# Optimization experiments

Measured on AMD Instinct MI355X. Metric: run time of the kernel, lower is better.

## Reference

```python
import jax, jax.numpy as jnp
import numpy as np

B, T, D, H = 2, 2048, 1024, 16
STD = 0.02

def setup_inputs() -> dict:
    key = jax.random.key(0)
    ks = jax.random.split(key, 5)
    x = jax.random.normal(ks[0], (B, T, D), dtype=jnp.float32)
    Wq = jax.random.normal(ks[1], (D, D), dtype=jnp.float32) * STD
    Wk = jax.random.normal(ks[2], (D, D), dtype=jnp.float32) * STD
    Wv = jax.random.normal(ks[3], (D, D), dtype=jnp.float32) * STD
    Wo = jax.random.normal(ks[4], (D, D), dtype=jnp.float32) * STD
    z = jnp.zeros((D,), dtype=jnp.float32)
    return {"x": x, "Wq": Wq, "bq": z, "Wk": Wk, "bk": z, "Wv": Wv, "bv": z, "Wo": Wo, "bo": z}

def _split(t, h):
    b, s, dm = t.shape
    return t.reshape(b, s, h, dm // h).transpose(0, 2, 1, 3)  # (B,h,T,d)

def reference(x, Wq, bq, Wk, bk, Wv, bv, Wo, bo):
    h = H
    # linear projections (nn.Linear: y = x @ W^T + b)
    q = _split(x @ Wq.T + bq, h)
    k = _split(x @ Wk.T + bk, h)
    v = _split(x @ Wv.T + bv, h)
    d_k = k.shape[-1]
    # scaled dot-product similarities (B,h,T,T)
    sim = jnp.einsum("bhqd,bhkd->bhqk", q, k) / jnp.sqrt(jnp.float32(d_k))
    # causal mask: upper triangle (excluding diag) filled with -inf
    Tq = sim.shape[-1]
    causal = jnp.tril(jnp.ones((Tq, Tq), dtype=bool))
    sim = jnp.where(causal, sim, -jnp.inf)
    attn = jax.nn.softmax(sim, axis=-1)
    ctx = jnp.einsum("bhqk,bhkd->bhqd", attn, v)  # (B,h,T,d)
    ctx = ctx.transpose(0, 2, 1, 3).reshape(x.shape[0], x.shape[1], -1)  # (B,T,D)
    return ctx @ Wo.T + bo
```

## Files before the change

kernel.cpp:

```cpp
#include <hip/hip_runtime.h>
#include <hip/hip_bf16.h>


typedef __attribute__((ext_vector_type(8))) short bf16x8;
typedef __attribute__((ext_vector_type(4))) float f32x4;

#define QSCALE 0.18033688011f

__device__ __forceinline__ int sniff_f32(const void* p) {
    const unsigned short* u = (const unsigned short*)p;
    int c = 0;
    for (int i = 0; i < 256; ++i) {
        int e = (u[i] >> 7) & 0xFF;
        c += (e >= 0x90) ? 1 : 0;
    }
    return c > 8;
}

__device__ __forceinline__ void async_copy16(const void* g, void* l) {
    __builtin_amdgcn_global_load_lds(
        (const __attribute__((address_space(1))) void*)g,
        (__attribute__((address_space(3))) void*)l, 16, 0, 0);
}

struct Cvt { const void* src; __hip_bfloat16* dst; int n; };
struct CvtPack { Cvt a[9]; };

__global__ __launch_bounds__(256) void cvt_bf16(CvtPack pk) {
    const Cvt c = pk.a[blockIdx.y];
    const int f32 = sniff_f32(c.src);
    const int stride = gridDim.x * 256 * 8;
    for (int idx = (blockIdx.x * 256 + threadIdx.x) * 8; idx < c.n; idx += stride) {
        if (f32) {
            const float* s = (const float*)c.src + idx;
            f32x4 a0 = *(const f32x4*)s;
            f32x4 a1 = *(const f32x4*)(s + 4);
            union { __hip_bfloat16 h[8]; bf16x8 v; } u;
#pragma unroll
            for (int e = 0; e < 4; e++) u.h[e]     = (__hip_bfloat16)a0[e];
#pragma unroll
            for (int e = 0; e < 4; e++) u.h[4 + e] = (__hip_bfloat16)a1[e];
            *(bf16x8*)&c.dst[idx] = u.v;
        } else {
            *(bf16x8*)&c.dst[idx] = *(const bf16x8*)((const __hip_bfloat16*)c.src + idx);
        }
    }
}

template <bool OF32>
__device__ __forceinline__ void gemm_async_body(
    const __hip_bfloat16* __restrict__ A, const __hip_bfloat16* __restrict__ W,
    const __hip_bfloat16* __restrict__ bias, void* __restrict__ C,
    int M, int N, int K, int bm, int bn, float outscale,
    __hip_bfloat16* sA, __hip_bfloat16* sB)
{
    const int tid  = threadIdx.x;
    const int wave = tid >> 6;
    const int lane = tid & 63;
    const int quad = lane >> 4;
    const int l15  = lane & 15;
    const int wr   = wave >> 1;
    const int wc   = wave & 1;

    const int srow = wave * 16 + (lane >> 2);
    const int scol = (lane & 3) * 8;
    const __hip_bfloat16* gA0 = A + (size_t)(bm + srow) * K + scol;
    const __hip_bfloat16* gB0 = W + (size_t)(bn + srow) * K + scol;
    __hip_bfloat16* sA0 = sA + wave * 512;
    __hip_bfloat16* sB0 = sB + wave * 512;

    f32x4 acc[4][4];
#pragma unroll
    for (int i = 0; i < 4; i++)
#pragma unroll
        for (int j = 0; j < 4; j++) acc[i][j] = (f32x4)0.0f;

    for (int k0 = 0; k0 < K; k0 += 32) {
        __syncthreads();
#pragma unroll
        for (int r = 0; r < 2; r++) {
            async_copy16(gA0 + (size_t)r * 64 * K + k0, sA0 + r * 2048);
            async_copy16(gB0 + (size_t)r * 64 * K + k0, sB0 + r * 2048);
        }
        __syncthreads();

        bf16x8 af[4], bf[4];
#pragma unroll
        for (int i = 0; i < 4; i++)
            af[i] = *(const bf16x8*)&sA[(wr * 64 + i * 16 + l15) * 32 + quad * 8];
#pragma unroll
        for (int j = 0; j < 4; j++)
            bf[j] = *(const bf16x8*)&sB[(wc * 64 + j * 16 + l15) * 32 + quad * 8];
#pragma unroll
        for (int i = 0; i < 4; i++)
#pragma unroll
            for (int j = 0; j < 4; j++)
                acc[i][j] = __builtin_amdgcn_mfma_f32_16x16x32_bf16(af[i], bf[j], acc[i][j], 0, 0, 0);
    }

    float bv[4];
#pragma unroll
    for (int j = 0; j < 4; j++)
        bv[j] = (float)bias[bn + wc * 64 + j * 16 + l15];
#pragma unroll
    for (int i = 0; i < 4; i++) {
#pragma unroll
        for (int j = 0; j < 4; j++) {
            int col = bn + wc * 64 + j * 16 + l15;
#pragma unroll
            for (int r = 0; r < 4; r++) {
                int row = bm + wr * 64 + i * 16 + quad * 4 + r;
                float v = (acc[i][j][r] + bv[j]) * outscale;
                if (OF32) ((float*)C)[(size_t)row * N + col] = v;
                else      ((__hip_bfloat16*)C)[(size_t)row * N + col] = (__hip_bfloat16)v;
            }
        }
    }
}

__global__ __launch_bounds__(256, 2) void qkv_gemm(
    const __hip_bfloat16* __restrict__ x,
    const __hip_bfloat16* __restrict__ Wq, const __hip_bfloat16* __restrict__ bq, __hip_bfloat16* __restrict__ Q,
    const __hip_bfloat16* __restrict__ Wk, const __hip_bfloat16* __restrict__ bk, __hip_bfloat16* __restrict__ Kb,
    const __hip_bfloat16* __restrict__ Wv, const __hip_bfloat16* __restrict__ bv, __hip_bfloat16* __restrict__ V,
    int M, int N, int K)
{
    __shared__ __hip_bfloat16 sA[128 * 32];
    __shared__ __hip_bfloat16 sB[128 * 32];
    const __hip_bfloat16* Wp; const __hip_bfloat16* bp; __hip_bfloat16* Cp; float sc;
    if (blockIdx.z == 0)      { Wp = Wq; bp = bq; Cp = Q;  sc = QSCALE; }
    else if (blockIdx.z == 1) { Wp = Wk; bp = bk; Cp = Kb; sc = 1.0f; }
    else                      { Wp = Wv; bp = bv; Cp = V;  sc = 1.0f; }
    gemm_async_body<false>(x, Wp, bp, Cp, M, N, K,
                           blockIdx.x * 128, blockIdx.y * 128, sc, sA, sB);
}

template <bool OF32>
__device__ __forceinline__ void gemm64_body(
    const __hip_bfloat16* __restrict__ A, const __hip_bfloat16* __restrict__ W,
    const __hip_bfloat16* __restrict__ bias, void* __restrict__ C,
    int M, int N, int K, int bm, int bn,
    __hip_bfloat16* sA, __hip_bfloat16* sB)
{
    const int tid  = threadIdx.x;
    const int wave = tid >> 6;
    const int lane = tid & 63;
    const int quad = lane >> 4;
    const int l15  = lane & 15;

    const int srow = wave * 16 + (lane >> 2);
    const int scol = (lane & 3) * 8;
    const __hip_bfloat16* gA0 = A + (size_t)(bm + srow) * K + scol;
    const __hip_bfloat16* gB0 = W + (size_t)(bn + srow) * K + scol;
    __hip_bfloat16* sA0 = sA + wave * 512;
    __hip_bfloat16* sB0 = sB + wave * 512;

    f32x4 acc[4][2];
#pragma unroll
    for (int i = 0; i < 4; i++)
#pragma unroll
        for (int j = 0; j < 2; j++) acc[i][j] = (f32x4)0.0f;

    for (int k0 = 0; k0 < K; k0 += 32) {
        __syncthreads();
        async_copy16(gA0 + k0, sA0);
#pragma unroll
        for (int r = 0; r < 2; r++)
            async_copy16(gB0 + (size_t)r * 64 * K + k0, sB0 + r * 2048);
        __syncthreads();

        bf16x8 af[4], bf[2];
#pragma unroll
        for (int i = 0; i < 4; i++)
            af[i] = *(const bf16x8*)&sA[(i * 16 + l15) * 32 + quad * 8];
#pragma unroll
        for (int j = 0; j < 2; j++)
            bf[j] = *(const bf16x8*)&sB[(wave * 32 + j * 16 + l15) * 32 + quad * 8];
#pragma unroll
        for (int i = 0; i < 4; i++)
#pragma unroll
            for (int j = 0; j < 2; j++)
                acc[i][j] = __builtin_amdgcn_mfma_f32_16x16x32_bf16(af[i], bf[j], acc[i][j], 0, 0, 0);
    }

    float bv[2];
#pragma unroll
    for (int j = 0; j < 2; j++)
        bv[j] = (float)bias[bn + wave * 32 + j * 16 + l15];
#pragma unroll
    for (int i = 0; i < 4; i++) {
#pragma unroll
        for (int j = 0; j < 2; j++) {
            int col = bn + wave * 32 + j * 16 + l15;
#pragma unroll
            for (int r = 0; r < 4; r++) {
                int row = bm + i * 16 + quad * 4 + r;
                float v = acc[i][j][r] + bv[j];
                if (OF32) ((float*)C)[(size_t)row * N + col] = v;
                else      ((__hip_bfloat16*)C)[(size_t)row * N + col] = (__hip_bfloat16)v;
            }
        }
    }
}

__global__ __launch_bounds__(256, 2) void out_gemm(
    const __hip_bfloat16* __restrict__ A, const __hip_bfloat16* __restrict__ W,
    const __hip_bfloat16* __restrict__ bias, const void* __restrict__ origW,
    void* __restrict__ C, int M, int N, int K)
{
    __shared__ __hip_bfloat16 sA[64 * 32];
    __shared__ __hip_bfloat16 sB[128 * 32];
    __shared__ int f32flag;
    if (threadIdx.x == 0) f32flag = sniff_f32(origW);
    __syncthreads();
    if (f32flag)
        gemm64_body<true>(A, W, bias, C, M, N, K, blockIdx.x * 64, blockIdx.y * 128, sA, sB);
    else
        gemm64_body<false>(A, W, bias, C, M, N, K, blockIdx.x * 64, blockIdx.y * 128, sA, sB);
}

__global__ __launch_bounds__(256, 2) void transpose_v(
    const __hip_bfloat16* __restrict__ V, __hip_bfloat16* __restrict__ VT,
    int T, int D, int H)
{
    __shared__ __hip_bfloat16 sT[64 * 72];
    const int tid = threadIdx.x;
    const int t0  = blockIdx.x * 64;
    const int h   = blockIdx.y;
    const int b   = blockIdx.z;

    for (int i = tid; i < 512; i += 256) {
        int t = i >> 3, d8 = (i & 7) * 8;
        *(bf16x8*)&sT[t * 72 + d8] =
            *(const bf16x8*)&V[((size_t)b * T + t0 + t) * D + h * 64 + d8];
    }
    __syncthreads();
    for (int i = tid; i < 512; i += 256) {
        int d = i >> 3, t8 = (i & 7) * 8;
        union { __hip_bfloat16 h[8]; bf16x8 v; } u;
#pragma unroll
        for (int e = 0; e < 8; e++) u.h[e] = sT[(t8 + e) * 72 + d];
        *(bf16x8*)&VT[(((size_t)b * H + h) * 64 + d) * T + t0 + t8] = u.v;
    }
}

#define PAD 68

__global__ __launch_bounds__(256, 2) void attn_causal(
    const __hip_bfloat16* __restrict__ Q,
    const __hip_bfloat16* __restrict__ K,
    const __hip_bfloat16* __restrict__ VT,
    __hip_bfloat16* __restrict__ O,
    int T, int D, int H)
{
    __shared__ __hip_bfloat16 sK[64 * PAD];
    __shared__ __hip_bfloat16 sVT[64 * PAD];
    __shared__ __hip_bfloat16 sP[4][32 * PAD];

    const int tid  = threadIdx.x;
    const int wave = tid >> 6;
    const int lane = tid & 63;
    const int quad = lane >> 4;
    const int l15  = lane & 15;

    const int NT = T >> 7;
    const int qt = blockIdx.z ? (NT - 1 - (int)blockIdx.x) : (int)blockIdx.x;
    const int h  = blockIdx.y;
    const int b  = blockIdx.z;
    const size_t headoff = (size_t)b * T * D + (size_t)h * 64;
    const size_t vtoff   = ((size_t)b * H + h) * 64 * (size_t)T;

    const int nkt = 2 * qt + 2;
    const int myrowmax = qt * 128 + wave * 32 + 31;

    bf16x8 qfrag[2][2];
#pragma unroll
    for (int g = 0; g < 2; g++)
#pragma unroll
        for (int kk = 0; kk < 2; kk++)
            qfrag[g][kk] = *(const bf16x8*)&Q[headoff +
                (size_t)(qt * 128 + wave * 32 + g * 16 + l15) * D + kk * 32 + quad * 8];

    f32x4 acc_o[2][4];
#pragma unroll
    for (int g = 0; g < 2; g++)
#pragma unroll
        for (int j = 0; j < 4; j++) acc_o[g][j] = (f32x4)0.0f;
    float lacc[2][4] = {{0.f,0.f,0.f,0.f},{0.f,0.f,0.f,0.f}};

    const int srow = tid >> 3;
    const int sc8  = (tid & 7) * 8;

    bf16x8 pk[2], pv[2];
#pragma unroll
    for (int u = 0; u < 2; u++) {
        int row = srow + u * 32;
        pk[u] = *(const bf16x8*)&K[headoff + (size_t)row * D + sc8];
        pv[u] = *(const bf16x8*)&VT[vtoff + (size_t)row * T + sc8];
    }

    for (int kt = 0; kt < nkt; ++kt) {
        __syncthreads();
#pragma unroll
        for (int u = 0; u < 2; u++) {
            int row = srow + u * 32;
            *(bf16x8*)&sK[row * PAD + sc8]  = pk[u];
            *(bf16x8*)&sVT[row * PAD + sc8] = pv[u];
        }
        if (kt + 1 < nkt) {
#pragma unroll
            for (int u = 0; u < 2; u++) {
                int row = srow + u * 32;
                pk[u] = *(const bf16x8*)&K[headoff + (size_t)((kt + 1) * 64 + row) * D + sc8];
                pv[u] = *(const bf16x8*)&VT[vtoff + (size_t)row * T + (kt + 1) * 64 + sc8];
            }
        }
        __syncthreads();

        if (kt * 64 > myrowmax) continue;

        bf16x8 kfrag[2][4], vfrag[2][4];
#pragma unroll
        for (int kk = 0; kk < 2; kk++)
#pragma unroll
            for (int j = 0; j < 4; j++) {
                kfrag[kk][j] = *(const bf16x8*)&sK[(j * 16 + l15) * PAD + kk * 32 + quad * 8];
                vfrag[kk][j] = *(const bf16x8*)&sVT[(j * 16 + l15) * PAD + kk * 32 + quad * 8];
            }

        const int needmask = (kt * 64 + 63 > qt * 128 + wave * 32 + quad * 4);

#pragma unroll
        for (int g = 0; g < 2; g++) {
            f32x4 s[4];
#pragma unroll
            for (int j = 0; j < 4; j++) s[j] = (f32x4)0.0f;
#pragma unroll
            for (int kk = 0; kk < 2; kk++)
#pragma unroll
                for (int j = 0; j < 4; j++)
                    s[j] = __builtin_amdgcn_mfma_f32_16x16x32_bf16(qfrag[g][kk], kfrag[kk][j], s[j], 0, 0, 0);

            if (needmask) {
                const int qrow = qt * 128 + wave * 32 + g * 16 + quad * 4;
#pragma unroll
                for (int j = 0; j < 4; j++) {
                    int key = kt * 64 + j * 16 + l15;
#pragma unroll
                    for (int r = 0; r < 4; r++)
                        if (key > qrow + r) s[j][r] = -1e30f;
                }
            }

#pragma unroll
            for (int j = 0; j < 4; j++) {
#pragma unroll
                for (int r = 0; r < 4; r++) {
                    float p = exp2f(s[j][r]);
                    lacc[g][r] += p;
                    sP[wave][(g * 16 + quad * 4 + r) * PAD + j * 16 + l15] = (__hip_bfloat16)p;
                }
            }
        }
#pragma unroll
        for (int g = 0; g < 2; g++)
#pragma unroll
            for (int kk = 0; kk < 2; kk++) {
                bf16x8 a = *(const bf16x8*)&sP[wave][(g * 16 + l15) * PAD + kk * 32 + quad * 8];
#pragma unroll
                for (int j = 0; j < 4; j++)
                    acc_o[g][j] = __builtin_amdgcn_mfma_f32_16x16x32_bf16(a, vfrag[kk][j], acc_o[g][j], 0, 0, 0);
            }
    }

#pragma unroll
    for (int o = 1; o < 16; o <<= 1)
#pragma unroll
        for (int g = 0; g < 2; g++)
#pragma unroll
            for (int r = 0; r < 4; r++)
                lacc[g][r] += __shfl_xor(lacc[g][r], o, 64);

#pragma unroll
    for (int g = 0; g < 2; g++)
#pragma unroll
        for (int r = 0; r < 4; r++) {
            float inv = 1.0f / lacc[g][r];
            int row = qt * 128 + wave * 32 + g * 16 + quad * 4 + r;
#pragma unroll
            for (int j = 0; j < 4; j++) {
                int col = j * 16 + l15;
                O[headoff + (size_t)row * D + col] = (__hip_bfloat16)(acc_o[g][j][r] * inv);
            }
        }
}

extern "C" void kernel_launch(void* const* d_in, const int* in_sizes, int n_in,
                              void* d_out, int out_size, void* d_ws, size_t ws_size,
                              hipStream_t stream) {
    const int Bb = 2, T = 2048, D = 1024, H = 16;
    const int M = Bb * T;

    __hip_bfloat16* w = (__hip_bfloat16*)d_ws;
    __hip_bfloat16* Q   = w;
    __hip_bfloat16* Kb  = Q   + (size_t)M * D;
    __hip_bfloat16* Vb  = Kb  + (size_t)M * D;
    __hip_bfloat16* ctx = Vb  + (size_t)M * D;
    __hip_bfloat16* VT  = ctx + (size_t)M * D;
    __hip_bfloat16* xb  = VT  + (size_t)M * D;
    __hip_bfloat16* Wqb = xb  + (size_t)M * D;
    __hip_bfloat16* Wkb = Wqb + (size_t)D * D;
    __hip_bfloat16* Wvb = Wkb + (size_t)D * D;
    __hip_bfloat16* Wob = Wvb + (size_t)D * D;
    __hip_bfloat16* bqb = Wob + (size_t)D * D;
    __hip_bfloat16* bkb = bqb + D;
    __hip_bfloat16* bvb = bkb + D;
    __hip_bfloat16* bob = bvb + D;

    CvtPack pk;
    pk.a[0] = { d_in[0], xb,  M * D };
    pk.a[1] = { d_in[1], Wqb, D * D };
    pk.a[2] = { d_in[2], bqb, D };
    pk.a[3] = { d_in[3], Wkb, D * D };
    pk.a[4] = { d_in[4], bkb, D };
    pk.a[5] = { d_in[5], Wvb, D * D };
    pk.a[6] = { d_in[6], bvb, D };
    pk.a[7] = { d_in[7], Wob, D * D };
    pk.a[8] = { d_in[8], bob, D };

    cvt_bf16<<<dim3(512, 9), 256, 0, stream>>>(pk);
    qkv_gemm<<<dim3(M / 128, D / 128, 3), 256, 0, stream>>>(
        xb, Wqb, bqb, Q, Wkb, bkb, Kb, Wvb, bvb, Vb, M, D, D);
    transpose_v<<<dim3(T / 64, H, Bb), 256, 0, stream>>>(Vb, VT, T, D, H);
    attn_causal<<<dim3(T / 128, H, Bb), 256, 0, stream>>>(Q, Kb, VT, ctx, T, D, H);
    out_gemm<<<dim3(M / 64, D / 128), 256, 0, stream>>>(
        ctx, Wob, bob, d_in[7], d_out, M, D, D);
}
```

Measured before the change: 222.9 us.

## Fuse V transpose into QKV GEMM epilogue and double-buffer attention K/V tiles

The V projection epilogue now writes V directly in the transposed per-head layout, which removes the separate transpose_v kernel and its extra round trip through global memory. The attention kernel double-buffers K and V^T in shared memory so only one barrier is needed per tile. It also computes S transposed (K as the A operand), which allows vectorized 4-wide stores of P and a per-lane row-sum reduction with fewer shuffles. The cost is twice the shared memory for the K/V tiles and scattered 8-byte stores in the V epilogue.

```diff
diff --git a/kernel.cpp b/kernel.cpp
--- a/kernel.cpp
+++ b/kernel.cpp
@@ -4,6 +4,7 @@
 
 typedef __attribute__((ext_vector_type(8))) short bf16x8;
 typedef __attribute__((ext_vector_type(4))) float f32x4;
+typedef __attribute__((ext_vector_type(4))) short s16x4;
 
 #define QSCALE 0.18033688011f
 
@@ -47,7 +48,7 @@
     }
 }
 
-template <bool OF32>
+template <int MODE>
 __device__ __forceinline__ void gemm_async_body(
     const __hip_bfloat16* __restrict__ A, const __hip_bfloat16* __restrict__ W,
     const __hip_bfloat16* __restrict__ bias, void* __restrict__ C,
@@ -102,17 +103,37 @@
 #pragma unroll
     for (int j = 0; j < 4; j++)
         bv[j] = (float)bias[bn + wc * 64 + j * 16 + l15];
-#pragma unroll
-    for (int i = 0; i < 4; i++) {
-#pragma unroll
-        for (int j = 0; j < 4; j++) {
-            int col = bn + wc * 64 + j * 16 + l15;
-#pragma unroll
-            for (int r = 0; r < 4; r++) {
-                int row = bm + wr * 64 + i * 16 + quad * 4 + r;
-                float v = (acc[i][j][r] + bv[j]) * outscale;
-                if (OF32) ((float*)C)[(size_t)row * N + col] = v;
-                else      ((__hip_bfloat16*)C)[(size_t)row * N + col] = (__hip_bfloat16)v;
+
+    if (MODE == 2) {
+        __hip_bfloat16* VTo = (__hip_bfloat16*)C;
+#pragma unroll
+        for (int i = 0; i < 4; i++) {
+            int tglob = bm + wr * 64 + i * 16 + quad * 4;
+            int bb = tglob >> 11, tt = tglob & 2047;
+#pragma unroll
+            for (int j = 0; j < 4; j++) {
+                int d = bn + wc * 64 + j * 16 + l15;
+                int hh = d >> 6, dh = d & 63;
+                union { __hip_bfloat16 e[4]; s16x4 v; } u;
+#pragma unroll
+                for (int r = 0; r < 4; r++)
+                    u.e[r] = (__hip_bfloat16)(acc[i][j][r] + bv[j]);
+                *(s16x4*)&VTo[(((size_t)bb * 16 + hh) * 64 + dh) * 2048 + tt] = u.v;
+            }
+        }
+    } else {
+#pragma unroll
+        for (int i = 0; i < 4; i++) {
+#pragma unroll
+            for (int j = 0; j < 4; j++) {
+                int col = bn + wc * 64 + j * 16 + l15;
+#pragma unroll
+                for (int r = 0; r < 4; r++) {
+                    int row = bm + wr * 64 + i * 16 + quad * 4 + r;
+                    float v = (acc[i][j][r] + bv[j]) * outscale;
+                    if (MODE == 1) ((float*)C)[(size_t)row * N + col] = v;
+                    else ((__hip_bfloat16*)C)[(size_t)row * N + col] = (__hip_bfloat16)v;
+                }
             }
         }
     }
@@ -122,17 +143,17 @@
     const __hip_bfloat16* __restrict__ x,
     const __hip_bfloat16* __restrict__ Wq, const __hip_bfloat16* __restrict__ bq, __hip_bfloat16* __restrict__ Q,
     const __hip_bfloat16* __restrict__ Wk, const __hip_bfloat16* __restrict__ bk, __hip_bfloat16* __restrict__ Kb,
-    const __hip_bfloat16* __restrict__ Wv, const __hip_bfloat16* __restrict__ bv, __hip_bfloat16* __restrict__ V,
+    const __hip_bfloat16* __restrict__ Wv, const __hip_bfloat16* __restrict__ bv, __hip_bfloat16* __restrict__ VT,
     int M, int N, int K)
 {
     __shared__ __hip_bfloat16 sA[128 * 32];
     __shared__ __hip_bfloat16 sB[128 * 32];
-    const __hip_bfloat16* Wp; const __hip_bfloat16* bp; __hip_bfloat16* Cp; float sc;
-    if (blockIdx.z == 0)      { Wp = Wq; bp = bq; Cp = Q;  sc = QSCALE; }
-    else if (blockIdx.z == 1) { Wp = Wk; bp = bk; Cp = Kb; sc = 1.0f; }
-    else                      { Wp = Wv; bp = bv; Cp = V;  sc = 1.0f; }
-    gemm_async_body<false>(x, Wp, bp, Cp, M, N, K,
-                           blockIdx.x * 128, blockIdx.y * 128, sc, sA, sB);
+    if (blockIdx.z == 0)
+        gemm_async_body<0>(x, Wq, bq, Q, M, N, K, blockIdx.x * 128, blockIdx.y * 128, QSCALE, sA, sB);
+    else if (blockIdx.z == 1)
+        gemm_async_body<0>(x, Wk, bk, Kb, M, N, K, blockIdx.x * 128, blockIdx.y * 128, 1.0f, sA, sB);
+    else
+        gemm_async_body<2>(x, Wv, bv, VT, M, N, K, blockIdx.x * 128, blockIdx.y * 128, 1.0f, sA, sB);
 }
 
 template <bool OF32>
@@ -219,31 +240,6 @@
         gemm64_body<false>(A, W, bias, C, M, N, K, blockIdx.x * 64, blockIdx.y * 128, sA, sB);
 }
 
-__global__ __launch_bounds__(256, 2) void transpose_v(
-    const __hip_bfloat16* __restrict__ V, __hip_bfloat16* __restrict__ VT,
-    int T, int D, int H)
-{
-    __shared__ __hip_bfloat16 sT[64 * 72];
-    const int tid = threadIdx.x;
-    const int t0  = blockIdx.x * 64;
-    const int h   = blockIdx.y;
-    const int b   = blockIdx.z;
-
-    for (int i = tid; i < 512; i += 256) {
-        int t = i >> 3, d8 = (i & 7) * 8;
-        *(bf16x8*)&sT[t * 72 + d8] =
-            *(const bf16x8*)&V[((size_t)b * T + t0 + t) * D + h * 64 + d8];
-    }
-    __syncthreads();
-    for (int i = tid; i < 512; i += 256) {
-        int d = i >> 3, t8 = (i & 7) * 8;
-        union { __hip_bfloat16 h[8]; bf16x8 v; } u;
-#pragma unroll
-        for (int e = 0; e < 8; e++) u.h[e] = sT[(t8 + e) * 72 + d];
-        *(bf16x8*)&VT[(((size_t)b * H + h) * 64 + d) * T + t0 + t8] = u.v;
-    }
-}
-
 #define PAD 68
 
 __global__ __launch_bounds__(256, 2) void attn_causal(
@@ -253,9 +249,9 @@
     __hip_bfloat16* __restrict__ O,
     int T, int D, int H)
 {
-    __shared__ __hip_bfloat16 sK[64 * PAD];
-    __shared__ __hip_bfloat16 sVT[64 * PAD];
-    __shared__ __hip_bfloat16 sP[4][32 * PAD];
+    __shared__ __hip_bfloat16 sK[2][64 * PAD];
+    __shared__ __hip_bfloat16 sVT[2][64 * PAD];
+    __shared__ __hip_bfloat16 sPA[4][32 * PAD];
 
     const int tid  = threadIdx.x;
     const int wave = tid >> 6;
@@ -286,7 +282,7 @@
     for (int g = 0; g < 2; g++)
 #pragma unroll
         for (int j = 0; j < 4; j++) acc_o[g][j] = (f32x4)0.0f;
-    float lacc[2][4] = {{0.f,0.f,0.f,0.f},{0.f,0.f,0.f,0.f}};
+    float lacc[2] = {0.f, 0.f};
 
     const int srow = tid >> 3;
     const int sc8  = (tid & 7) * 8;
@@ -298,99 +294,119 @@
         pk[u] = *(const bf16x8*)&K[headoff + (size_t)row * D + sc8];
         pv[u] = *(const bf16x8*)&VT[vtoff + (size_t)row * T + sc8];
     }
-
-    for (int kt = 0; kt < nkt; ++kt) {
-        __syncthreads();
+#pragma unroll
+    for (int u = 0; u < 2; u++) {
+        int row = srow + u * 32;
+        *(bf16x8*)&sK[0][row * PAD + sc8]  = pk[u];
+        *(bf16x8*)&sVT[0][row * PAD + sc8] = pv[u];
+    }
+    if (nkt > 1) {
 #pragma unroll
         for (int u = 0; u < 2; u++) {
             int row = srow + u * 32;
-            *(bf16x8*)&sK[row * PAD + sc8]  = pk[u];
-            *(bf16x8*)&sVT[row * PAD + sc8] = pv[u];
-        }
+            pk[u] = *(const bf16x8*)&K[headoff + (size_t)(64 + row) * D + sc8];
+            pv[u] = *(const bf16x8*)&VT[vtoff + (size_t)row * T + 64 + sc8];
+        }
+    }
+    __syncthreads();
+
+    for (int kt = 0; kt < nkt; ++kt) {
+        const int cur = kt & 1;
+
         if (kt + 1 < nkt) {
 #pragma unroll
             for (int u = 0; u < 2; u++) {
                 int row = srow + u * 32;
-                pk[u] = *(const bf16x8*)&K[headoff + (size_t)((kt + 1) * 64 + row) * D + sc8];
-                pv[u] = *(const bf16x8*)&VT[vtoff + (size_t)row * T + (kt + 1) * 64 + sc8];
-            }
-        }
+                *(bf16x8*)&sK[1 - cur][row * PAD + sc8]  = pk[u];
+                *(bf16x8*)&sVT[1 - cur][row * PAD + sc8] = pv[u];
+            }
+            if (kt + 2 < nkt) {
+#pragma unroll
+                for (int u = 0; u < 2; u++) {
+                    int row = srow + u * 32;
+                    pk[u] = *(const bf16x8*)&K[headoff + (size_t)((kt + 2) * 64 + row) * D + sc8];
+                    pv[u] = *(const bf16x8*)&VT[vtoff + (size_t)row * T + (kt + 2) * 64 + sc8];
+                }
+            }
+        }
+
+        if (kt * 64 <= myrowmax) {
+            bf16x8 kfrag[2][4], vfrag[2][4];
+#pragma unroll
+            for (int kk = 0; kk < 2; kk++)
+#pragma unroll
+                for (int j = 0; j < 4; j++) {
+                    kfrag[kk][j] = *(const bf16x8*)&sK[cur][(j * 16 + l15) * PAD + kk * 32 + quad * 8];
+                    vfrag[kk][j] = *(const bf16x8*)&sVT[cur][(j * 16 + l15) * PAD + kk * 32 + quad * 8];
+                }
+
+#pragma unroll
+            for (int g = 0; g < 2; g++) {
+                const int qbase = qt * 128 + wave * 32 + g * 16;
+                f32x4 st[4];
+#pragma unroll
+                for (int j = 0; j < 4; j++) st[j] = (f32x4)0.0f;
+#pragma unroll
+                for (int kk = 0; kk < 2; kk++)
+#pragma unroll
+                    for (int j = 0; j < 4; j++)
+                        st[j] = __builtin_amdgcn_mfma_f32_16x16x32_bf16(
+                            kfrag[kk][j], qfrag[g][kk], st[j], 0, 0, 0);
+
+                if (kt * 64 + 63 > qbase) {
+                    const int q = qbase + l15;
+#pragma unroll
+                    for (int j = 0; j < 4; j++) {
+                        int keyb = kt * 64 + j * 16 + quad * 4;
+#pragma unroll
+                        for (int r = 0; r < 4; r++)
+                            if (keyb + r > q) st[j][r] = -1e30f;
+                    }
+                }
+
+#pragma unroll
+                for (int j = 0; j < 4; j++) {
+                    union { __hip_bfloat16 e[4]; s16x4 v; } u;
+#pragma unroll
+                    for (int r = 0; r < 4; r++) {
+                        float p = exp2f(st[j][r]);
+                        lacc[g] += p;
+                        u.e[r] = (__hip_bfloat16)p;
+                    }
+                    *(s16x4*)&sPA[wave][(g * 16 + l15) * PAD + j * 16 + quad * 4] = u.v;
+                }
+            }
+#pragma unroll
+            for (int g = 0; g < 2; g++)
+#pragma unroll
+                for (int kk = 0; kk < 2; kk++) {
+                    bf16x8 a = *(const bf16x8*)&sPA[wave][(g * 16 + l15) * PAD + kk * 32 + quad * 8];
+#pragma unroll
+                    for (int j = 0; j < 4; j++)
+                        acc_o[g][j] = __builtin_amdgcn_mfma_f32_16x16x32_bf16(
+                            a, vfrag[kk][j], acc_o[g][j], 0, 0, 0);
+                }
+        }
+
         __syncthreads();
-
-        if (kt * 64 > myrowmax) continue;
-
-        bf16x8 kfrag[2][4], vfrag[2][4];
-#pragma unroll
-        for (int kk = 0; kk < 2; kk++)
-#pragma unroll
-            for (int j = 0; j < 4; j++) {
-                kfrag[kk][j] = *(const bf16x8*)&sK[(j * 16 + l15) * PAD + kk * 32 + quad * 8];
-                vfrag[kk][j] = *(const bf16x8*)&sVT[(j * 16 + l15) * PAD + kk * 32 + quad * 8];
-            }
-
-        const int needmask = (kt * 64 + 63 > qt * 128 + wave * 32 + quad * 4);
-
-#pragma unroll
-        for (int g = 0; g < 2; g++) {
-            f32x4 s[4];
-#pragma unroll
-            for (int j = 0; j < 4; j++) s[j] = (f32x4)0.0f;
-#pragma unroll
-            for (int kk = 0; kk < 2; kk++)
-#pragma unroll
-                for (int j = 0; j < 4; j++)
-                    s[j] = __builtin_amdgcn_mfma_f32_16x16x32_bf16(qfrag[g][kk], kfrag[kk][j], s[j], 0, 0, 0);
-
-            if (needmask) {
-                const int qrow = qt * 128 + wave * 32 + g * 16 + quad * 4;
-#pragma unroll
-                for (int j = 0; j < 4; j++) {
-                    int key = kt * 64 + j * 16 + l15;
-#pragma unroll
-                    for (int r = 0; r < 4; r++)
-                        if (key > qrow + r) s[j][r] = -1e30f;
-                }
-            }
-
-#pragma unroll
-            for (int j = 0; j < 4; j++) {
-#pragma unroll
-                for (int r = 0; r < 4; r++) {
-                    float p = exp2f(s[j][r]);
-                    lacc[g][r] += p;
-                    sP[wave][(g * 16 + quad * 4 + r) * PAD + j * 16 + l15] = (__hip_bfloat16)p;
-                }
-            }
-        }
-#pragma unroll
-        for (int g = 0; g < 2; g++)
-#pragma unroll
-            for (int kk = 0; kk < 2; kk++) {
-                bf16x8 a = *(const bf16x8*)&sP[wave][(g * 16 + l15) * PAD + kk * 32 + quad * 8];
-#pragma unroll
-                for (int j = 0; j < 4; j++)
-                    acc_o[g][j] = __builtin_amdgcn_mfma_f32_16x16x32_bf16(a, vfrag[kk][j], acc_o[g][j], 0, 0, 0);
-            }
-    }
-
-#pragma unroll
-    for (int o = 1; o < 16; o <<= 1)
-#pragma unroll
-        for (int g = 0; g < 2; g++)
-#pragma unroll
-            for (int r = 0; r < 4; r++)
-                lacc[g][r] += __shfl_xor(lacc[g][r], o, 64);
+    }
+
+#pragma unroll
+    for (int g = 0; g < 2; g++) {
+        lacc[g] += __shfl_xor(lacc[g], 16, 64);
+        lacc[g] += __shfl_xor(lacc[g], 32, 64);
+    }
 
 #pragma unroll
     for (int g = 0; g < 2; g++)
 #pragma unroll
         for (int r = 0; r < 4; r++) {
-            float inv = 1.0f / lacc[g][r];
+            float linv = 1.0f / __shfl(lacc[g], quad * 4 + r, 64);
             int row = qt * 128 + wave * 32 + g * 16 + quad * 4 + r;
 #pragma unroll
             for (int j = 0; j < 4; j++) {
                 int col = j * 16 + l15;
-                O[headoff + (size_t)row * D + col] = (__hip_bfloat16)(acc_o[g][j][r] * inv);
+                O[headoff + (size_t)row * D + col] = (__hip_bfloat16)(acc_o[g][j][r] * linv);
             }
         }
 }
@@ -404,10 +420,9 @@
     __hip_bfloat16* w = (__hip_bfloat16*)d_ws;
     __hip_bfloat16* Q   = w;
     __hip_bfloat16* Kb  = Q   + (size_t)M * D;
-    __hip_bfloat16* Vb  = Kb  + (size_t)M * D;
-    __hip_bfloat16* ctx = Vb  + (size_t)M * D;
-    __hip_bfloat16* VT  = ctx + (size_t)M * D;
-    __hip_bfloat16* xb  = VT  + (size_t)M * D;
+    __hip_bfloat16* VT  = Kb  + (size_t)M * D;
+    __hip_bfloat16* ctx = VT  + (size_t)M * D;
+    __hip_bfloat16* xb  = ctx + (size_t)M * D;
     __hip_bfloat16* Wqb = xb  + (size_t)M * D;
     __hip_bfloat16* Wkb = Wqb + (size_t)D * D;
     __hip_bfloat16* Wvb = Wkb + (size_t)D * D;
@@ -430,8 +445,7 @@
 
     cvt_bf16<<<dim3(512, 9), 256, 0, stream>>>(pk);
     qkv_gemm<<<dim3(M / 128, D / 128, 3), 256, 0, stream>>>(
-        xb, Wqb, bqb, Q, Wkb, bkb, Kb, Wvb, bvb, Vb, M, D, D);
-    transpose_v<<<dim3(T / 64, H, Bb), 256, 0, stream>>>(Vb, VT, T, D, H);
+        xb, Wqb, bqb, Q, Wkb, bkb, Kb, Wvb, bvb, VT, M, D, D);
     attn_causal<<<dim3(T / 128, H, Bb), 256, 0, stream>>>(Q, Kb, VT, ctx, T, D, H);
     out_gemm<<<dim3(M / 64, D / 128), 256, 0, stream>>>(
         ctx, Wob, bob, d_in[7], d_out, M, D, D);
```

Measured after the change: 213.6 us. 4.2% less time.
